# Kernel optimization log

Hardware: AMD Instinct MI355X
Metric: run time of the kernel (lower is better)

## Reference

```python
import jax, jax.numpy as jnp
import numpy as np

B, S, E, H, NQ = 8, 2048, 8, 2, 8
D = E // H  # head_dim = 4
DIM = 2 ** NQ  # 256-amplitude state vector

# CNOT chain pattern from the module: (0,1),(1,2),...,(NQ-2,NQ-1),(NQ-1,0)
CNOTS = [(i, i + 1) for i in range(NQ - 1)] + [(NQ - 1, 0)]

# Pauli-Z sign table: wire 0 is the most-significant qubit axis (torchquantum convention)
_k = np.arange(DIM)
_SIGNS = (1.0 - 2.0 * ((_k[None, :] >> (NQ - 1 - np.arange(NQ))[:, None]) & 1)).astype(np.float32)  # (NQ, DIM)


def _quantum_measure(tok):
    """Batched simulation of the per-token circuit. tok: (N, E) real -> (N, NQ) <Z> values."""
    n = tok.shape[0]
    idx = jnp.arange(NQ) % D
    # encoder RX(tok[w]) then explicit RX(tok[w % head_dim]) on each wire: angles add.
    half = 0.5 * (tok[:, :NQ] + tok[:, idx])  # (N, NQ)
    a0 = jnp.cos(half).astype(jnp.complex64)
    a1 = (-1j) * jnp.sin(half).astype(jnp.complex64)
    qub = jnp.stack([a0, a1], axis=-1)  # (N, NQ, 2) per-qubit states (product state before CNOTs)
    # Kronecker product across the fixed NQ wires
    state = qub[:, 0, :]
    for w in range(1, NQ):
        state = (state[:, :, None] * qub[:, w, None, :]).reshape(n, -1)
    state = state.reshape((n,) + (2,) * NQ)
    # CNOT chain: flip target axis within control=1 block
    for c, t in CNOTS:
        c0 = jax.lax.index_in_dim(state, 0, c + 1, keepdims=True)
        c1 = jnp.flip(jax.lax.index_in_dim(state, 1, c + 1, keepdims=True), axis=t + 1)
        state = jnp.concatenate([c0, c1], axis=c + 1)
    p = (state.real ** 2 + state.imag ** 2).reshape(n, DIM)  # probabilities
    return p @ jnp.asarray(_SIGNS.T)  # (N, NQ) Pauli-Z expectations


def setup_inputs() -> dict:
    key = jax.random.key(0)
    ks = jax.random.split(key, 5)
    sc = 1.0 / np.sqrt(E)
    return {
        "x": jax.random.normal(ks[0], (B, S, E), jnp.float32),
        "Wq": jax.random.normal(ks[1], (E, E), jnp.float32) * sc,
        "Wk": jax.random.normal(ks[2], (E, E), jnp.float32) * sc,
        "Wv": jax.random.normal(ks[3], (E, E), jnp.float32) * sc,
        "Wo": jax.random.normal(ks[4], (E, E), jnp.float32) * sc,
    }


def reference(x, Wq, Wk, Wv, Wo):
    b, s, _ = x.shape
    # nn.Linear(bias=False): y = x @ W^T
    q = jnp.einsum('bse,fe->bsf', x, Wq).reshape(b, s, H, D)
    k = jnp.einsum('bse,fe->bsf', x, Wk).reshape(b, s, H, D)
    v = jnp.einsum('bse,fe->bsf', x, Wv).reshape(b, s, H, D)
    scores = jnp.einsum('bihd,bjhd->bhij', q, k) / jnp.sqrt(jnp.float32(D))
    attn = jax.nn.softmax(scores, axis=-1)  # dropout is identity at inference
    out = jnp.einsum('bhij,bjhd->bihd', attn, v).reshape(b, s, E)
    z = _quantum_measure(out.reshape(-1, E)).reshape(b, s, NQ)  # NQ == E
    return jnp.einsum('bsq,fq->bsf', z, Wo)
```

## Files before the change

### kernel.cpp

```cpp
#include <hip/hip_runtime.h>


#define SS 2048
#define EE 8

typedef float v2f __attribute__((ext_vector_type(2)));

extern "C" __global__ __launch_bounds__(256, 8)
void qa_attn14(const float* __restrict__ x, const float* __restrict__ Wq,
               const float* __restrict__ Wk, const float* __restrict__ Wv,
               float* __restrict__ wsD, float4* __restrict__ wsA) {
    __shared__ float wrow[96];
    __shared__ __align__(16) float4 kv4[512];
    __shared__ float rden[3 * 128];
    __shared__ __align__(16) float4 racc[3 * 128];

    const int bid = blockIdx.x;
    const int jw = bid & 7, rt = (bid >> 3) & 15, h = (bid >> 7) & 1, b = bid >> 8;
    const int tid = threadIdx.x, lane = tid & 63, w = tid >> 6;

    if (tid < 96) {
        const int grp = tid >> 5, d = (tid >> 3) & 3, e = tid & 7;
        const float* W = (grp == 0) ? Wq : (grp == 1 ? Wk : Wv);
        float val = W[(h * 4 + d) * EE + e];
        if (grp == 0) val *= 0.72134752044f;
        wrow[tid] = val;
    }
    __syncthreads();

    {
        const int j = jw * 256 + tid;
        const float* xp = x + ((size_t)(b * SS + j)) * EE;
        float xv[8];
        *(float4*)&xv[0] = *(const float4*)xp;
        *(float4*)&xv[4] = *(const float4*)(xp + 4);
        float kk[4], vv[4];
        #pragma unroll
        for (int d = 0; d < 4; ++d) {
            float sk = 0.f, sv = 0.f;
            #pragma unroll
            for (int e = 0; e < 8; ++e) {
                sk += xv[e] * wrow[32 + d * 8 + e];
                sv += xv[e] * wrow[64 + d * 8 + e];
            }
            kk[d] = sk; vv[d] = sv;
        }
        kv4[tid * 2]     = make_float4(kk[0], kk[1], kk[2], kk[3]);
        kv4[tid * 2 + 1] = make_float4(vv[0], vv[1], vv[2], vv[3]);
    }

    float q[2][4];
    const int row0 = rt * 128 + lane;
    #pragma unroll
    for (int m = 0; m < 2; ++m) {
        const float* xp = x + ((size_t)(b * SS + row0 + m * 64)) * EE;
        float xv[8];
        *(float4*)&xv[0] = *(const float4*)xp;
        *(float4*)&xv[4] = *(const float4*)(xp + 4);
        #pragma unroll
        for (int d = 0; d < 4; ++d) {
            float s = 0.f;
            #pragma unroll
            for (int e = 0; e < 8; ++e) s += xv[e] * wrow[d * 8 + e];
            q[m][d] = s;
        }
    }
    __syncthreads();

    v2f qp[4];
    #pragma unroll
    for (int d = 0; d < 4; ++d) qp[d] = (v2f){q[0][d], q[1][d]};
    v2f denp = (v2f){0.f, 0.f};
    v2f accp[4];
    #pragma unroll
    for (int c = 0; c < 4; ++c) accp[c] = (v2f){0.f, 0.f};

    const float4* kvp = &kv4[w * 128];
    #pragma unroll 2
    for (int jl = 0; jl < 64; ++jl) {
        const float4 kk = kvp[jl * 2];
        const float4 vv = kvp[jl * 2 + 1];
        v2f s = qp[0] * (v2f){kk.x, kk.x};
        s = __builtin_elementwise_fma(qp[1], (v2f){kk.y, kk.y}, s);
        s = __builtin_elementwise_fma(qp[2], (v2f){kk.z, kk.z}, s);
        s = __builtin_elementwise_fma(qp[3], (v2f){kk.w, kk.w}, s);
        v2f e;
        e.x = __builtin_amdgcn_exp2f(s.x);
        e.y = __builtin_amdgcn_exp2f(s.y);
        denp += e;
        accp[0] = __builtin_elementwise_fma(e, (v2f){vv.x, vv.x}, accp[0]);
        accp[1] = __builtin_elementwise_fma(e, (v2f){vv.y, vv.y}, accp[1]);
        accp[2] = __builtin_elementwise_fma(e, (v2f){vv.z, vv.z}, accp[2]);
        accp[3] = __builtin_elementwise_fma(e, (v2f){vv.w, vv.w}, accp[3]);
    }

    float den[2] = {denp.x, denp.y};
    float acc[2][4];
    #pragma unroll
    for (int c = 0; c < 4; ++c) { acc[0][c] = accp[c].x; acc[1][c] = accp[c].y; }

    if (w > 0) {
        #pragma unroll
        for (int m = 0; m < 2; ++m) {
            rden[(w - 1) * 128 + lane + m * 64] = den[m];
            racc[(w - 1) * 128 + lane + m * 64] =
                make_float4(acc[m][0], acc[m][1], acc[m][2], acc[m][3]);
        }
    }
    __syncthreads();
    if (w == 0) {
        #pragma unroll
        for (int m = 0; m < 2; ++m) {
            const int r = lane + m * 64;
            float d = den[m] + rden[r] + rden[128 + r] + rden[256 + r];
            float4 a1 = racc[r], a2 = racc[128 + r], a3 = racc[256 + r];
            float4 a = make_float4(acc[m][0] + a1.x + a2.x + a3.x,
                                   acc[m][1] + a1.y + a2.y + a3.y,
                                   acc[m][2] + a1.z + a2.z + a3.z,
                                   acc[m][3] + a1.w + a2.w + a3.w);
            const size_t idx = ((size_t)((b * 2 + h) * 8 + jw)) * SS + row0 + m * 64;
            wsD[idx] = d;
            wsA[idx] = a;
        }
    }
}

extern "C" __global__ __launch_bounds__(256)
void qa_merge14(const float* __restrict__ wsD, const float4* __restrict__ wsA,
                const float* __restrict__ Wo, float* __restrict__ out) {
    __shared__ float wo[64];
    const int tid = threadIdx.x;
    if (tid < 64) wo[tid] = Wo[tid];
    __syncthreads();

    const int gt = blockIdx.x * 256 + tid;
    const int g = gt >> 1, h = gt & 1;
    const int b = g >> 11, s = g & 2047;

    float den = 0.f, a0 = 0.f, a1 = 0.f, a2 = 0.f, a3 = 0.f;
    #pragma unroll
    for (int sl = 0; sl < 8; ++sl) {
        const size_t idx = ((size_t)((b * 2 + h) * 8 + sl)) * SS + s;
        den += wsD[idx];
        const float4 p = wsA[idx];
        a0 += p.x; a1 += p.y; a2 += p.z; a3 += p.w;
    }
    const float inv = 1.f / den;
    float own[4] = {a0 * inv, a1 * inv, a2 * inv, a3 * inv};
    float oth[4];
    #pragma unroll
    for (int c = 0; c < 4; ++c) oth[c] = __shfl_xor(own[c], 1);

    float tok[8];
    #pragma unroll
    for (int c = 0; c < 4; ++c) {
        tok[c]     = h ? oth[c] : own[c];
        tok[4 + c] = h ? own[c] : oth[c];
    }

    float cc[8];
    #pragma unroll
    for (int ww = 0; ww < 8; ++ww) cc[ww] = __cosf(tok[ww] + tok[ww & 3]);

    float z[8];
    float p = 1.f;
    #pragma unroll
    for (int qq = 1; qq < 8; ++qq) { p *= cc[qq]; z[qq] = p; }
    z[0] = p;
    #pragma unroll
    for (int qq = 1; qq < 8; ++qq) z[qq] *= cc[0];

    float y[4];
    #pragma unroll
    for (int f = 0; f < 4; ++f) {
        float sum = 0.f;
        #pragma unroll
        for (int qq = 0; qq < 8; ++qq) sum += z[qq] * wo[(h * 4 + f) * 8 + qq];
        y[f] = sum;
    }
    float4* op = (float4*)(out + (size_t)g * 8) + h;
    *op = make_float4(y[0], y[1], y[2], y[3]);
}

extern "C" void kernel_launch(void* const* d_in, const int* in_sizes, int n_in,
                              void* d_out, int out_size, void* d_ws, size_t ws_size,
                              hipStream_t stream) {
    const float* x  = (const float*)d_in[0];
    const float* Wq = (const float*)d_in[1];
    const float* Wk = (const float*)d_in[2];
    const float* Wv = (const float*)d_in[3];
    const float* Wo = (const float*)d_in[4];
    float* out = (float*)d_out;

    float*  wsD = (float*)d_ws;
    float4* wsA = (float4*)((char*)d_ws + (16 * 8 * 2048) * sizeof(float));

    qa_attn14<<<dim3(2048), dim3(256), 0, stream>>>(x, Wq, Wk, Wv, wsD, wsA);
    qa_merge14<<<dim3(128), dim3(256), 0, stream>>>(wsD, wsA, Wo, out);
}
```

Before: 83.79 us.

## Precompute K/V in a prep kernel and read them via scalar constant loads

Adds a prep kernel that projects K and V once per token into a workspace, instead of every attention block recomputing them from x. The attention kernel then reads K/V through address-space-4 (constant/scalar) pointers with wave-uniform indices, so the loads can become scalar loads broadcast to the wave and the LDS staging plus one barrier go away. The cost is an extra launch and a global round trip for K/V. Scalar-load latency inside the inner loop could also stall the exp/FMA chain.

```diff
diff --git a/kernel.cpp b/kernel.cpp
--- a/kernel.cpp
+++ b/kernel.cpp
@@ -5,49 +5,61 @@
 #define EE 8
 
 typedef float v2f __attribute__((ext_vector_type(2)));
-
-extern "C" __global__ __launch_bounds__(256, 8)
-void qa_attn14(const float* __restrict__ x, const float* __restrict__ Wq,
-               const float* __restrict__ Wk, const float* __restrict__ Wv,
-               float* __restrict__ wsD, float4* __restrict__ wsA) {
-    __shared__ float wrow[96];
-    __shared__ __align__(16) float4 kv4[512];
-    __shared__ float rden[3 * 128];
-    __shared__ __align__(16) float4 racc[3 * 128];
-
-    const int bid = blockIdx.x;
-    const int jw = bid & 7, rt = (bid >> 3) & 15, h = (bid >> 7) & 1, b = bid >> 8;
-    const int tid = threadIdx.x, lane = tid & 63, w = tid >> 6;
-
-    if (tid < 96) {
-        const int grp = tid >> 5, d = (tid >> 3) & 3, e = tid & 7;
-        const float* W = (grp == 0) ? Wq : (grp == 1 ? Wk : Wv);
-        float val = W[(h * 4 + d) * EE + e];
-        if (grp == 0) val *= 0.72134752044f;
-        wrow[tid] = val;
-    }
-    __syncthreads();
-
-    {
-        const int j = jw * 256 + tid;
-        const float* xp = x + ((size_t)(b * SS + j)) * EE;
-        float xv[8];
-        *(float4*)&xv[0] = *(const float4*)xp;
-        *(float4*)&xv[4] = *(const float4*)(xp + 4);
-        float kk[4], vv[4];
+typedef __attribute__((address_space(4))) const float c4f;
+
+extern "C" __global__ __launch_bounds__(128)
+void qa_prep15(const float* __restrict__ x, const float* __restrict__ Wk,
+               const float* __restrict__ Wv, float4* __restrict__ kvws) {
+    __shared__ float wrow[128];
+    const int tid = threadIdx.x;
+    wrow[tid] = (tid < 64) ? Wk[tid] : Wv[tid - 64];
+    __syncthreads();
+
+    const int g = blockIdx.x * 128 + tid;
+    const int b = g >> 11, s = g & 2047;
+    const float* xp = x + (size_t)g * EE;
+    float xv[8];
+    *(float4*)&xv[0] = *(const float4*)xp;
+    *(float4*)&xv[4] = *(const float4*)(xp + 4);
+
+    #pragma unroll
+    for (int h = 0; h < 2; ++h) {
+        float kd[4], vd[4];
         #pragma unroll
         for (int d = 0; d < 4; ++d) {
+            const int r = (h * 4 + d) * 8;
             float sk = 0.f, sv = 0.f;
             #pragma unroll
             for (int e = 0; e < 8; ++e) {
-                sk += xv[e] * wrow[32 + d * 8 + e];
-                sv += xv[e] * wrow[64 + d * 8 + e];
+                sk += xv[e] * wrow[r + e];
+                sv += xv[e] * wrow[64 + r + e];
             }
-            kk[d] = sk; vv[d] = sv;
-        }
-        kv4[tid * 2]     = make_float4(kk[0], kk[1], kk[2], kk[3]);
-        kv4[tid * 2 + 1] = make_float4(vv[0], vv[1], vv[2], vv[3]);
-    }
+            kd[d] = sk; vd[d] = sv;
+        }
+        const size_t o = ((size_t)(b * 2 + h) * SS + s) * 2;
+        kvws[o]     = make_float4(kd[0], kd[1], kd[2], kd[3]);
+        kvws[o + 1] = make_float4(vd[0], vd[1], vd[2], vd[3]);
+    }
+}
+
+extern "C" __global__ __launch_bounds__(256, 8)
+void qa_attn15(const float* __restrict__ x, const float* __restrict__ Wq,
+               const float4* __restrict__ kvws,
+               float* __restrict__ wsD, float4* __restrict__ wsA) {
+    __shared__ float wrow[32];
+    __shared__ float rden[3 * 128];
+    __shared__ __align__(16) float4 racc[3 * 128];
+
+    const int bid = blockIdx.x;
+    const int jw = bid & 7, rt = (bid >> 3) & 15, h = (bid >> 7) & 1, b = bid >> 8;
+    const int tid = threadIdx.x, lane = tid & 63;
+    const int w = __builtin_amdgcn_readfirstlane(tid >> 6);
+
+    if (tid < 32) {
+        const int d = tid >> 3, e = tid & 7;
+        wrow[tid] = Wq[(h * 4 + d) * EE + e] * 0.72134752044f;
+    }
+    __syncthreads();
 
     float q[2][4];
     const int row0 = rt * 128 + lane;
@@ -65,7 +77,6 @@
             q[m][d] = s;
         }
     }
-    __syncthreads();
 
     v2f qp[4];
     #pragma unroll
@@ -75,23 +86,27 @@
     #pragma unroll
     for (int c = 0; c < 4; ++c) accp[c] = (v2f){0.f, 0.f};
 
-    const float4* kvp = &kv4[w * 128];
-    #pragma unroll 2
+    const size_t base = ((size_t)((b * 2 + h)) * SS + jw * 256 + w * 64) * 8;
+    const c4f* kvp = (const c4f*)(unsigned long long)((const float*)kvws + base);
+
+    #pragma unroll 4
     for (int jl = 0; jl < 64; ++jl) {
-        const float4 kk = kvp[jl * 2];
-        const float4 vv = kvp[jl * 2 + 1];
-        v2f s = qp[0] * (v2f){kk.x, kk.x};
-        s = __builtin_elementwise_fma(qp[1], (v2f){kk.y, kk.y}, s);
-        s = __builtin_elementwise_fma(qp[2], (v2f){kk.z, kk.z}, s);
-        s = __builtin_elementwise_fma(qp[3], (v2f){kk.w, kk.w}, s);
+        const float k0 = kvp[jl * 8 + 0], k1 = kvp[jl * 8 + 1];
+        const float k2 = kvp[jl * 8 + 2], k3 = kvp[jl * 8 + 3];
+        const float v0 = kvp[jl * 8 + 4], v1 = kvp[jl * 8 + 5];
+        const float v2 = kvp[jl * 8 + 6], v3 = kvp[jl * 8 + 7];
+        v2f s = qp[0] * (v2f){k0, k0};
+        s = __builtin_elementwise_fma(qp[1], (v2f){k1, k1}, s);
+        s = __builtin_elementwise_fma(qp[2], (v2f){k2, k2}, s);
+        s = __builtin_elementwise_fma(qp[3], (v2f){k3, k3}, s);
         v2f e;
         e.x = __builtin_amdgcn_exp2f(s.x);
         e.y = __builtin_amdgcn_exp2f(s.y);
         denp += e;
-        accp[0] = __builtin_elementwise_fma(e, (v2f){vv.x, vv.x}, accp[0]);
-        accp[1] = __builtin_elementwise_fma(e, (v2f){vv.y, vv.y}, accp[1]);
-        accp[2] = __builtin_elementwise_fma(e, (v2f){vv.z, vv.z}, accp[2]);
-        accp[3] = __builtin_elementwise_fma(e, (v2f){vv.w, vv.w}, accp[3]);
+        accp[0] = __builtin_elementwise_fma(e, (v2f){v0, v0}, accp[0]);
+        accp[1] = __builtin_elementwise_fma(e, (v2f){v1, v1}, accp[1]);
+        accp[2] = __builtin_elementwise_fma(e, (v2f){v2, v2}, accp[2]);
+        accp[3] = __builtin_elementwise_fma(e, (v2f){v3, v3}, accp[3]);
     }
 
     float den[2] = {denp.x, denp.y};
@@ -126,7 +141,7 @@
 }
 
 extern "C" __global__ __launch_bounds__(256)
-void qa_merge14(const float* __restrict__ wsD, const float4* __restrict__ wsA,
+void qa_merge15(const float* __restrict__ wsD, const float4* __restrict__ wsA,
                 const float* __restrict__ Wo, float* __restrict__ out) {
     __shared__ float wo[64];
     const int tid = threadIdx.x;
@@ -192,9 +207,11 @@
     const float* Wo = (const float*)d_in[4];
     float* out = (float*)d_out;
 
-    float*  wsD = (float*)d_ws;
-    float4* wsA = (float4*)((char*)d_ws + (16 * 8 * 2048) * sizeof(float));
-
-    qa_attn14<<<dim3(2048), dim3(256), 0, stream>>>(x, Wq, Wk, Wv, wsD, wsA);
-    qa_merge14<<<dim3(128), dim3(256), 0, stream>>>(wsD, wsA, Wo, out);
-}
+    float4* kvws = (float4*)d_ws;
+    float*  wsD  = (float*)((char*)d_ws + (1u << 20));
+    float4* wsA  = (float4*)((char*)d_ws + (2u << 20));
+
+    qa_prep15<<<dim3(128), dim3(128), 0, stream>>>(x, Wk, Wv, kvws);
+    qa_attn15<<<dim3(2048), dim3(256), 0, stream>>>(x, Wq, kvws, wsD, wsA);
+    qa_merge15<<<dim3(128), dim3(256), 0, stream>>>(wsD, wsA, Wo, out);
+}
```

After: 84.38 us. About the same (+0.7%).
